# Performance work log

Measured on AMD Instinct MI355X. Metric: run time of the kernel, lower is better.

Reference implementation:

```python
import jax, jax.numpy as jnp
import numpy as np

BATCH = 4096
INPUT_DIM = 8192
NUM_BLOCKS = 12
ALPHA = 0.9
W_SCALE = 0.7071  # pytorch Conv1d kaiming-uniform bound: sqrt(1/(in_ch*k)) = sqrt(1/2)


def setup_inputs() -> dict:
    key = jax.random.key(0)
    k0, k1, k2, k3, k4 = jax.random.split(key, 5)
    x = jax.random.normal(k0, (BATCH, INPUT_DIM), dtype=jnp.float32)
    w1 = jax.random.uniform(k1, (NUM_BLOCKS, 2), jnp.float32, -W_SCALE, W_SCALE)
    b1 = jax.random.uniform(k2, (NUM_BLOCKS,), jnp.float32, -W_SCALE, W_SCALE)
    w2 = jax.random.uniform(k3, (NUM_BLOCKS, 2), jnp.float32, -W_SCALE, W_SCALE)
    b2 = jax.random.uniform(k4, (NUM_BLOCKS,), jnp.float32, -W_SCALE, W_SCALE)
    return {"x": x, "w1": w1, "b1": b1, "w2": w2, "b2": b2}


def _block(x, w1, b1, w2, b2):
    # conv1: kernel 2, padding 1 -> length L+1; channel dim is size 1 so drop it.
    xp = jnp.pad(x, ((0, 0), (1, 1)))                       # [B, L+2]
    y = jax.nn.elu(w1[0] * xp[:, :-1] + w1[1] * xp[:, 1:] + b1)  # [B, L+1]
    # conv2: kernel 2, padding 0 -> length L
    z = w2[0] * y[:, :-1] + w2[1] * y[:, 1:] + b2            # [B, L]
    return x + ALPHA * z


def reference(x, w1, b1, w2, b2):
    def step(carry, params):
        pw1, pb1, pw2, pb2 = params
        return _block(carry, pw1, pb1, pw2, pb2), None

    out, _ = jax.lax.scan(step, x, (w1, b1, w2, b2))
    return out
```

## Files before the change

kernel.cpp:

```cpp
#include <hip/hip_runtime.h>

#define BATCH  4096
#define LEN    8192
#define NB     12
#define TPB    512
#define EPT    16

__device__ __forceinline__ float ep_f(float as) {
    const float LN2 = 0.6931471805599453f;
    float e = __builtin_amdgcn_exp2f(fminf(as, 0.0f));
    return fmaxf(e, fmaf(as, LN2, 1.0f));
}

__global__ __launch_bounds__(TPB, 8)
void resconv1d_kernel(const float* __restrict__ x_in,
                      const float* __restrict__ w1,
                      const float* __restrict__ b1,
                      const float* __restrict__ w2,
                      const float* __restrict__ b2,
                      float* __restrict__ out)
{
    __shared__ float s_first[2][TPB];
    __shared__ float s_last [2][TPB];
    __shared__ float s_w[NB][6];

    const int t   = threadIdx.x;
    const int row = blockIdx.x;

    const float* xp = x_in + (size_t)row * LEN + (size_t)t * EPT;
    float y[EPT];
    #pragma unroll
    for (int k = 0; k < EPT / 4; ++k) {
        float4 v = reinterpret_cast<const float4*>(xp)[k];
        y[4*k+0] = v.x; y[4*k+1] = v.y; y[4*k+2] = v.z; y[4*k+3] = v.w;
    }

    if (t < NB) {
        const float LOG2E = 1.4426950408889634f;
        const float aw20 = 0.9f * w2[2*t];
        const float aw21 = 0.9f * w2[2*t+1];
        s_w[t][0] = w1[2*t]   * LOG2E;
        s_w[t][1] = w1[2*t+1] * LOG2E;
        s_w[t][2] = b1[t]     * LOG2E;
        s_w[t][3] = aw20;
        s_w[t][4] = aw21;
        s_w[t][5] = 0.9f * b2[t] - aw20 - aw21;
    }

    const int  idxl = (t > 0)       ? t - 1 : 0;
    const int  idxr = (t < TPB - 1) ? t + 1 : TPB - 1;
    const bool at_l = (t == 0);
    const bool at_r = (t == TPB - 1);

    float D = 0.0f;

    #pragma unroll 1
    for (int it = 0; it < NB; ++it) {
        const int buf = it & 1;
        s_first[buf][t] = y[0];
        s_last [buf][t] = y[EPT-1];
        __syncthreads();

        const float w10s = s_w[it][0];
        const float w11s = s_w[it][1];
        const float b1sr = s_w[it][2];
        const float aw20 = s_w[it][3];
        const float aw21 = s_w[it][4];
        const float cc   = s_w[it][5];

        const float b1p = fmaf(-D, w10s + w11s, b1sr);

        const float yl = at_l ? D : s_last [buf][idxl];
        const float yr = at_r ? D : s_first[buf][idxr];

        float as0 = fmaf(w10s, yl, fmaf(w11s, y[0], b1p));
        float ep0 = ep_f(as0);
        #pragma unroll
        for (int j = 0; j < EPT; ++j) {
            const float yn  = (j < EPT - 1) ? y[j+1] : yr;
            const float as1 = fmaf(w10s, y[j], fmaf(w11s, yn, b1p));
            const float ep1 = ep_f(as1);
            y[j] = fmaf(aw20, ep0, fmaf(aw21, ep1, y[j]));
            ep0 = ep1;
        }
        D -= cc;
    }

    float* op = out + (size_t)row * LEN + (size_t)t * EPT;
    #pragma unroll
    for (int k = 0; k < EPT / 4; ++k) {
        float4 v = make_float4(y[4*k+0] - D, y[4*k+1] - D,
                               y[4*k+2] - D, y[4*k+3] - D);
        reinterpret_cast<float4*>(op)[k] = v;
    }
}

extern "C" void kernel_launch(void* const* d_in, const int* in_sizes, int n_in,
                              void* d_out, int out_size, void* d_ws, size_t ws_size,
                              hipStream_t stream) {
    const float* x  = (const float*)d_in[0];
    const float* w1 = (const float*)d_in[1];
    const float* b1 = (const float*)d_in[2];
    const float* w2 = (const float*)d_in[3];
    const float* b2 = (const float*)d_in[4];
    float* out = (float*)d_out;

    resconv1d_kernel<<<dim3(BATCH), dim3(TPB), 0, stream>>>(x, w1, b1, w2, b2, out);
}
```

Baseline: 115.8 us.

## Process each row with a single wavefront using shuffles instead of LDS halo exchange

Each row is now handled by one 64-lane wavefront with 128 elements per thread instead of 512 threads with 16 each. Neighbour halo values are exchanged with warp shuffles, which removes the per-iteration shared-memory writes and block-wide barriers. The cost is heavier register pressure from the 128-float per-thread array and fewer threads per row. Global loads are now strided by 512 bytes across lanes, which may hurt coalescing.

```diff
diff --git a/kernel.cpp b/kernel.cpp
--- a/kernel.cpp
+++ b/kernel.cpp
@@ -3,8 +3,8 @@
 #define BATCH  4096
 #define LEN    8192
 #define NB     12
-#define TPB    512
-#define EPT    16
+#define TPB    64
+#define EPT    128
 
 __device__ __forceinline__ float ep_f(float as) {
     const float LN2 = 0.6931471805599453f;
@@ -12,7 +12,7 @@
     return fmaxf(e, fmaf(as, LN2, 1.0f));
 }
 
-__global__ __launch_bounds__(TPB, 8)
+__global__ __launch_bounds__(TPB, 3)
 void resconv1d_kernel(const float* __restrict__ x_in,
                       const float* __restrict__ w1,
                       const float* __restrict__ b1,
@@ -20,14 +20,12 @@
                       const float* __restrict__ b2,
                       float* __restrict__ out)
 {
-    __shared__ float s_first[2][TPB];
-    __shared__ float s_last [2][TPB];
     __shared__ float s_w[NB][6];
 
-    const int t   = threadIdx.x;
-    const int row = blockIdx.x;
+    const int lane = threadIdx.x;
+    const int row  = blockIdx.x;
 
-    const float* xp = x_in + (size_t)row * LEN + (size_t)t * EPT;
+    const float* xp = x_in + (size_t)row * LEN + (size_t)lane * EPT;
     float y[EPT];
     #pragma unroll
     for (int k = 0; k < EPT / 4; ++k) {
@@ -35,32 +33,26 @@
         y[4*k+0] = v.x; y[4*k+1] = v.y; y[4*k+2] = v.z; y[4*k+3] = v.w;
     }
 
-    if (t < NB) {
+    if (lane < NB) {
         const float LOG2E = 1.4426950408889634f;
-        const float aw20 = 0.9f * w2[2*t];
-        const float aw21 = 0.9f * w2[2*t+1];
-        s_w[t][0] = w1[2*t]   * LOG2E;
-        s_w[t][1] = w1[2*t+1] * LOG2E;
-        s_w[t][2] = b1[t]     * LOG2E;
-        s_w[t][3] = aw20;
-        s_w[t][4] = aw21;
-        s_w[t][5] = 0.9f * b2[t] - aw20 - aw21;
+        const float aw20 = 0.9f * w2[2*lane];
+        const float aw21 = 0.9f * w2[2*lane+1];
+        s_w[lane][0] = w1[2*lane]   * LOG2E;
+        s_w[lane][1] = w1[2*lane+1] * LOG2E;
+        s_w[lane][2] = b1[lane]     * LOG2E;
+        s_w[lane][3] = aw20;
+        s_w[lane][4] = aw21;
+        s_w[lane][5] = 0.9f * b2[lane] - aw20 - aw21;
     }
+    __syncthreads();
 
-    const int  idxl = (t > 0)       ? t - 1 : 0;
-    const int  idxr = (t < TPB - 1) ? t + 1 : TPB - 1;
-    const bool at_l = (t == 0);
-    const bool at_r = (t == TPB - 1);
+    const bool at_l = (lane == 0);
+    const bool at_r = (lane == TPB - 1);
 
     float D = 0.0f;
 
     #pragma unroll 1
     for (int it = 0; it < NB; ++it) {
-        const int buf = it & 1;
-        s_first[buf][t] = y[0];
-        s_last [buf][t] = y[EPT-1];
-        __syncthreads();
-
         const float w10s = s_w[it][0];
         const float w11s = s_w[it][1];
         const float b1sr = s_w[it][2];
@@ -68,10 +60,12 @@
         const float aw21 = s_w[it][4];
         const float cc   = s_w[it][5];
 
+        float yl = __shfl_up  (y[EPT-1], 1, 64);
+        float yr = __shfl_down(y[0],     1, 64);
+        yl = at_l ? D : yl;
+        yr = at_r ? D : yr;
+
         const float b1p = fmaf(-D, w10s + w11s, b1sr);
-
-        const float yl = at_l ? D : s_last [buf][idxl];
-        const float yr = at_r ? D : s_first[buf][idxr];
 
         float as0 = fmaf(w10s, yl, fmaf(w11s, y[0], b1p));
         float ep0 = ep_f(as0);
@@ -86,7 +80,7 @@
         D -= cc;
     }
 
-    float* op = out + (size_t)row * LEN + (size_t)t * EPT;
+    float* op = out + (size_t)row * LEN + (size_t)lane * EPT;
     #pragma unroll
     for (int k = 0; k < EPT / 4; ++k) {
         float4 v = make_float4(y[4*k+0] - D, y[4*k+1] - D,
```

New measurement: 119.5 us. 1.03x slower.

## Replace exp2-based ELU with clamped polynomial and double elements per thread

Applied to the files above, without the earlier changes.

The per-element ELU term is now evaluated with a degree-6 polynomial on a clamped, rescaled argument plus a linear branch, in place of the hardware exp2 instruction. The weights are prescaled to match the polynomial's domain. Blocks shrink to 256 threads with 32 elements each, which halves the shared-memory halo exchange per element. The polynomial swaps a transcendental instruction for several full-rate FMAs, but it adds approximation error and saturates for very negative inputs. The larger per-thread register array may also lower occupancy.

```diff
diff --git a/kernel.cpp b/kernel.cpp
--- a/kernel.cpp
+++ b/kernel.cpp
@@ -3,13 +3,24 @@
 #define BATCH  4096
 #define LEN    8192
 #define NB     12
-#define TPB    512
-#define EPT    16
+#define TPB    256
+#define EPT    32
 
-__device__ __forceinline__ float ep_f(float as) {
-    const float LN2 = 0.6931471805599453f;
-    float e = __builtin_amdgcn_exp2f(fminf(as, 0.0f));
-    return fmaxf(e, fmaf(as, LN2, 1.0f));
+__device__ __forceinline__ float ep_poly(float v) {
+    const float C0 = 0.0152109f, C1 = 0.0764958f, C2 = 0.1480698f,
+                C3 = 0.0993620f, C4 = 0.1326600f, C5 = 0.3221584f,
+                C6 = 0.2037216f;
+    const float SIXLN2   =  4.1588831f;
+    const float ONEM6LN2 = -3.1588831f;
+    float u = __builtin_amdgcn_fmed3f(v, -1.0f, 1.0f);
+    float p = fmaf(C6, u, C5);
+    p = fmaf(p, u, C4);
+    p = fmaf(p, u, C3);
+    p = fmaf(p, u, C2);
+    p = fmaf(p, u, C1);
+    p = fmaf(p, u, C0);
+    float lin = fmaf(v, SIXLN2, ONEM6LN2);
+    return fmaxf(p, lin);
 }
 
 __global__ __launch_bounds__(TPB, 8)
@@ -36,12 +47,12 @@
     }
 
     if (t < NB) {
-        const float LOG2E = 1.4426950408889634f;
+        const float L6 = 0.2404491734814939f;
         const float aw20 = 0.9f * w2[2*t];
         const float aw21 = 0.9f * w2[2*t+1];
-        s_w[t][0] = w1[2*t]   * LOG2E;
-        s_w[t][1] = w1[2*t+1] * LOG2E;
-        s_w[t][2] = b1[t]     * LOG2E;
+        s_w[t][0] = w1[2*t]   * L6;
+        s_w[t][1] = w1[2*t+1] * L6;
+        s_w[t][2] = fmaf(b1[t], L6, 1.0f);
         s_w[t][3] = aw20;
         s_w[t][4] = aw21;
         s_w[t][5] = 0.9f * b2[t] - aw20 - aw21;
@@ -73,13 +84,13 @@
         const float yl = at_l ? D : s_last [buf][idxl];
         const float yr = at_r ? D : s_first[buf][idxr];
 
-        float as0 = fmaf(w10s, yl, fmaf(w11s, y[0], b1p));
-        float ep0 = ep_f(as0);
+        float v0  = fmaf(w10s, yl, fmaf(w11s, y[0], b1p));
+        float ep0 = ep_poly(v0);
         #pragma unroll
         for (int j = 0; j < EPT; ++j) {
             const float yn  = (j < EPT - 1) ? y[j+1] : yr;
-            const float as1 = fmaf(w10s, y[j], fmaf(w11s, yn, b1p));
-            const float ep1 = ep_f(as1);
+            const float v1  = fmaf(w10s, y[j], fmaf(w11s, yn, b1p));
+            const float ep1 = ep_poly(v1);
             y[j] = fmaf(aw20, ep0, fmaf(aw21, ep1, y[j]));
             ep0 = ep1;
         }
```

Measured after the change: 127.6 us. 1.1x slower.
